# Optimization experiments

Hardware: AMD Instinct MI355X
Metric: run time of the kernel (lower is better)

Reference implementation:

```python
import jax, jax.numpy as jnp
import numpy as np

B, T, M, D, H, DK, DV = 2, 1024, 1024, 1024, 16, 64, 64
R = 2 * T + M  # number of relative positions required by rel_shift path


def setup_inputs() -> dict:
    key = jax.random.key(0)
    ks = jax.random.split(key, 11)
    s = 0.02
    return {
        "inputs": jax.random.normal(ks[0], (B, T, D), jnp.float32),
        "attention_mask": jnp.ones((B, T, M + T), jnp.float32),
        "positional_encodings": jax.random.normal(ks[1], (R, D), jnp.float32),
        "memory": jax.random.normal(ks[2], (B, M, D), jnp.float32),
        "Wq": jax.random.normal(ks[3], (D, H * DK), jnp.float32) * s,
        "Wk": jax.random.normal(ks[4], (D, H * DK), jnp.float32) * s,
        "Wv": jax.random.normal(ks[5], (D, H * DV), jnp.float32) * s,
        "Wr": jax.random.normal(ks[6], (D, H * DK), jnp.float32) * s,
        "r_w_bias": jax.random.normal(ks[7], (H, DK), jnp.float32) * s,
        "r_r_bias": jax.random.normal(ks[8], (H, DK), jnp.float32) * s,
        "W_out": jax.random.normal(ks[9], (H * DV, D), jnp.float32) * s,
    }


def _rel_shift(m, attention_length):
    # m: [T_q, T_q + L] -> [T_q, L], TXL relative shift via reshape/slice
    tq, total = m.shape
    x = m.reshape(total, tq)[1:].reshape(tq, total - 1)
    return x[:, :attention_length]


def reference(inputs, attention_mask, positional_encodings, memory,
              Wq, Wk, Wv, Wr, r_w_bias, r_r_bias, W_out):
    b, t, d = inputs.shape
    values = jnp.concatenate([memory, inputs], axis=1)  # [B, L, D]
    L = values.shape[1]
    q = (inputs @ Wq).reshape(b, t, H, DK)
    k = (values @ Wk).reshape(b, L, H, DK)
    v = (values @ Wv).reshape(b, L, H, DV)
    rk = (positional_encodings @ Wr).reshape(-1, H, DK)  # [R, H, DK]
    # content + relative logits (TXL)
    content = jnp.einsum('bthd,bThd->bhtT', q + r_w_bias, k)        # [B,H,T,L]
    rel = jnp.einsum('bthd,rhd->bhtr', q + r_r_bias, rk)            # [B,H,T,R]
    rel = jax.vmap(jax.vmap(lambda m: _rel_shift(m, L)))(rel)       # [B,H,T,L]
    logits = (content + rel) * (DK ** -0.5)
    masked = logits - (1.0 - attention_mask[:, None, :, :]) * 1e30
    w = jax.nn.softmax(masked, axis=-1)
    attn = jnp.einsum('bhtT,bThd->bthd', w, v)                      # [B,T,H,DV]
    return attn.reshape(b, t, H * DV) @ W_out
```

## Files before the change

### kernel.cpp

```cpp
#include <hip/hip_runtime.h>
#include <hip/hip_fp16.h>
#include <stdint.h>

#define Bz 2
#define Tq 1024
#define Mm 1024
#define Hh 16
#define Ll 2048
#define Rr 3072

typedef __attribute__((ext_vector_type(8))) short bf16x8;
typedef __attribute__((ext_vector_type(4))) float f32x4;

typedef __attribute__((address_space(3))) uint8_t lds_u8_t;
typedef __attribute__((address_space(1))) uint8_t glb_u8_t;

__device__ __forceinline__ void gl2lds16(const void* g, void* l) {
  __builtin_amdgcn_global_load_lds((const glb_u8_t*)g, (lds_u8_t*)l, 16, 0, 0);
}

__device__ __forceinline__ unsigned short f2bf(float f) {
  unsigned int u = __builtin_bit_cast(unsigned int, f);
  u = u + 0x7fffu + ((u >> 16) & 1u);
  return (unsigned short)(u >> 16);
}
__device__ __forceinline__ float b2f(unsigned short s) {
  unsigned int u = ((unsigned int)s) << 16;
  return __builtin_bit_cast(float, u);
}

__global__ __launch_bounds__(256) void k_prep2(
    const float* __restrict__ x, const float* __restrict__ mem,
    const float* __restrict__ pos, const float* __restrict__ mask,
    const float* __restrict__ w0, const float* __restrict__ w1,
    const float* __restrict__ w2, const float* __restrict__ w3,
    const float* __restrict__ w4,
    unsigned short* __restrict__ vin, unsigned short* __restrict__ pb,
    unsigned short* __restrict__ mb,
    unsigned short* __restrict__ t0, unsigned short* __restrict__ t1,
    unsigned short* __restrict__ t2, unsigned short* __restrict__ t3,
    unsigned short* __restrict__ t4) {
  __shared__ float tile[64][65];
  int bid = blockIdx.x;
  if (bid < 4096) {
    int idx = bid * 256 + threadIdx.x;
    int e = idx << 2;
    int row = e >> 10, col = e & 1023;
    int b = row >> 11, l = row & 2047;
    const float* s = (l < Mm) ? (mem + (((size_t)b * Mm + l) << 10) + col)
                              : (x + (((size_t)b * Tq + (l - Mm)) << 10) + col);
    float4 v = *(const float4*)s;
    ushort4 o;
    o.x = f2bf(v.x); o.y = f2bf(v.y); o.z = f2bf(v.z); o.w = f2bf(v.w);
    *(ushort4*)(vin + e) = o;
  } else if (bid < 7168) {
    int idx = (bid - 4096) * 256 + threadIdx.x;
    int e = idx << 2;
    float4 v = *(const float4*)(pos + e);
    ushort4 t;
    t.x = f2bf(v.x); t.y = f2bf(v.y); t.z = f2bf(v.z); t.w = f2bf(v.w);
    *(ushort4*)(pb + e) = t;
  } else if (bid < 11264) {
    int idx = (bid - 7168) * 256 + threadIdx.x;
    int e = idx << 2;
    const float BIGM = 1.442695e30f;
    float4 v = *(const float4*)(mask + e);
    ushort4 t;
    t.x = f2bf((1.0f - v.x) * BIGM); t.y = f2bf((1.0f - v.y) * BIGM);
    t.z = f2bf((1.0f - v.z) * BIGM); t.w = f2bf((1.0f - v.w) * BIGM);
    *(ushort4*)(mb + e) = t;
  } else {
    int r3 = bid - 11264;
    int mz = r3 >> 8, rem = r3 & 255;
    const float* W;
    unsigned short* WT;
    switch (mz) {
      case 0: W = w0; WT = t0; break;
      case 1: W = w1; WT = t1; break;
      case 2: W = w2; WT = t2; break;
      case 3: W = w3; WT = t3; break;
      default: W = w4; WT = t4; break;
    }
    int k0 = (rem >> 4) * 64, n0 = (rem & 15) * 64;
    int tid = threadIdx.x;
    int rr = tid >> 4, c4 = (tid & 15) * 4;
#pragma unroll
    for (int it = 0; it < 4; ++it) {
      int r = rr + it * 16;
      float4 v = *(const float4*)(W + (size_t)(k0 + r) * 1024 + n0 + c4);
      tile[r][c4] = v.x; tile[r][c4 + 1] = v.y;
      tile[r][c4 + 2] = v.z; tile[r][c4 + 3] = v.w;
    }
    __syncthreads();
#pragma unroll
    for (int it = 0; it < 4; ++it) {
      int n = rr + it * 16;
      ushort4 o;
      o.x = f2bf(tile[c4 + 0][n]); o.y = f2bf(tile[c4 + 1][n]);
      o.z = f2bf(tile[c4 + 2][n]); o.w = f2bf(tile[c4 + 3][n]);
      *(ushort4*)(WT + (size_t)(n0 + n) * 1024 + k0 + c4) = o;
    }
  }
}

template <int RMAP>
__device__ __forceinline__ void gemm_core(const unsigned short* __restrict__ A,
                                          const unsigned short* __restrict__ Bt,
                                          int m0, int n0, unsigned short* As,
                                          unsigned short* Bs, f32x4 acc[4][4]) {
  const int tid = threadIdx.x;
  const int w = tid >> 6, lane = tid & 63;
  const int quad = lane >> 4, li = lane & 15;
  const int wr = w >> 1, wc = w & 1;
  f32x4 z = {0.f, 0.f, 0.f, 0.f};
#pragma unroll
  for (int mi = 0; mi < 4; ++mi)
#pragma unroll
    for (int ni = 0; ni < 4; ++ni) acc[mi][ni] = z;

  const int rs = lane >> 2;
  const int cs = lane & 3;

  for (int k0 = 0; k0 < 1024; k0 += 32) {
    __syncthreads();
#pragma unroll
    for (int s = 0; s < 2; ++s) {
      int i = w * 2 + s;
      int r = i * 16 + rs;
      int c = cs ^ ((r >> 1) & 3);
      int ar = m0 + r;
      if (RMAP) ar = ar + 1024 + (ar & 1024);
      gl2lds16(A + (size_t)ar * 1024 + k0 + c * 8, (char*)As + i * 1024);
      int br = n0 + r;
      gl2lds16(Bt + (size_t)br * 1024 + k0 + c * 8, (char*)Bs + i * 1024);
    }
    __syncthreads();
    bf16x8 af[4], bfr[4];
#pragma unroll
    for (int mi = 0; mi < 4; ++mi) {
      int r = wr * 64 + mi * 16 + li;
      int ch = quad ^ ((r >> 1) & 3);
      af[mi] = *(const bf16x8*)((const char*)As + r * 64 + ch * 16);
    }
#pragma unroll
    for (int ni = 0; ni < 4; ++ni) {
      int r = wc * 64 + ni * 16 + li;
      int ch = quad ^ ((r >> 1) & 3);
      bfr[ni] = *(const bf16x8*)((const char*)Bs + r * 64 + ch * 16);
    }
#pragma unroll
    for (int mi = 0; mi < 4; ++mi)
#pragma unroll
      for (int ni = 0; ni < 4; ++ni)
        acc[mi][ni] = __builtin_amdgcn_mfma_f32_16x16x32_bf16(
            af[mi], bfr[ni], acc[mi][ni], 0, 0, 0);
  }
}

__global__ __launch_bounds__(256, 2) void k_proj(
    const unsigned short* __restrict__ Vin, const unsigned short* __restrict__ Pb,
    const unsigned short* __restrict__ WqT, const unsigned short* __restrict__ WkT,
    const unsigned short* __restrict__ WvT, const unsigned short* __restrict__ WrT,
    unsigned short* __restrict__ qb, unsigned short* __restrict__ kb,
    unsigned short* __restrict__ vtb, unsigned short* __restrict__ rkb) {
  __shared__ unsigned short As[128 * 32];
  __shared__ unsigned short Bs[128 * 32];
  __shared__ unsigned short Bs2[128 * 32];
  const int t = blockIdx.x;
  const int tid = threadIdx.x, w = tid >> 6, lane = tid & 63;
  const int quad = lane >> 4, li = lane & 15, wr = w >> 1, wc = w & 1;
  f32x4 z = {0.f, 0.f, 0.f, 0.f};

  if (t < 256) {
    int m0 = (t >> 3) * 128, n0 = (t & 7) * 128;
    f32x4 ak[4][4], av[4][4];
#pragma unroll
    for (int mi = 0; mi < 4; ++mi)
#pragma unroll
      for (int ni = 0; ni < 4; ++ni) { ak[mi][ni] = z; av[mi][ni] = z; }
    const int rs = lane >> 2, cs = lane & 3;
    for (int k0 = 0; k0 < 1024; k0 += 32) {
      __syncthreads();
#pragma unroll
      for (int s = 0; s < 2; ++s) {
        int i = w * 2 + s;
        int r = i * 16 + rs;
        int c = cs ^ ((r >> 1) & 3);
        gl2lds16(Vin + (size_t)(m0 + r) * 1024 + k0 + c * 8, (char*)As + i * 1024);
        gl2lds16(WkT + (size_t)(n0 + r) * 1024 + k0 + c * 8, (char*)Bs + i * 1024);
        gl2lds16(WvT + (size_t)(n0 + r) * 1024 + k0 + c * 8, (char*)Bs2 + i * 1024);
      }
      __syncthreads();
      bf16x8 af[4], bk[4], bv[4];
#pragma unroll
      for (int mi = 0; mi < 4; ++mi) {
        int r = wr * 64 + mi * 16 + li;
        int ch = quad ^ ((r >> 1) & 3);
        af[mi] = *(const bf16x8*)((const char*)As + r * 64 + ch * 16);
      }
#pragma unroll
      for (int ni = 0; ni < 4; ++ni) {
        int r = wc * 64 + ni * 16 + li;
        int ch = quad ^ ((r >> 1) & 3);
        bk[ni] = *(const bf16x8*)((const char*)Bs + r * 64 + ch * 16);
        bv[ni] = *(const bf16x8*)((const char*)Bs2 + r * 64 + ch * 16);
      }
#pragma unroll
      for (int mi = 0; mi < 4; ++mi)
#pragma unroll
        for (int ni = 0; ni < 4; ++ni) {
          ak[mi][ni] = __builtin_amdgcn_mfma_f32_16x16x32_bf16(
              af[mi], bk[ni], ak[mi][ni], 0, 0, 0);
          av[mi][ni] = __builtin_amdgcn_mfma_f32_16x16x32_bf16(
              af[mi], bv[ni], av[mi][ni], 0, 0, 0);
        }
    }
#pragma unroll
    for (int mi = 0; mi < 4; ++mi)
#pragma unroll
      for (int ni = 0; ni < 4; ++ni) {
        int cc = n0 + wc * 64 + ni * 16 + li;
#pragma unroll
        for (int reg = 0; reg < 4; ++reg) {
          int rrow = m0 + wr * 64 + mi * 16 + quad * 4 + reg;
          kb[(size_t)rrow * 1024 + cc] = f2bf(ak[mi][ni][reg]);
        }
        int r0 = m0 + wr * 64 + mi * 16 + quad * 4;
        int b = r0 >> 11, l0 = r0 & 2047;
        ushort4 o;
        o.x = f2bf(av[mi][ni][0]); o.y = f2bf(av[mi][ni][1]);
        o.z = f2bf(av[mi][ni][2]); o.w = f2bf(av[mi][ni][3]);
        *(ushort4*)(vtb + ((size_t)(b * 1024 + cc)) * Ll + l0) = o;
      }
  } else if (t < 384) {
    int tt = t - 256;
    int m0 = (tt >> 3) * 128, n0 = (tt & 7) * 128;
    f32x4 acc[4][4];
    gemm_core<1>(Vin, WqT, m0, n0, As, Bs, acc);
#pragma unroll
    for (int mi = 0; mi < 4; ++mi)
#pragma unroll
      for (int ni = 0; ni < 4; ++ni)
#pragma unroll
        for (int reg = 0; reg < 4; ++reg) {
          int rrow = m0 + wr * 64 + mi * 16 + quad * 4 + reg;
          int cc = n0 + wc * 64 + ni * 16 + li;
          qb[(size_t)rrow * 1024 + cc] = f2bf(acc[mi][ni][reg]);
        }
  } else {
    int tt = t - 384;
    int m0 = (tt >> 3) * 128, n0 = (tt & 7) * 128;
    f32x4 acc[4][4];
    gemm_core<0>(Pb, WrT, m0, n0, As, Bs, acc);
#pragma unroll
    for (int mi = 0; mi < 4; ++mi)
#pragma unroll
      for (int ni = 0; ni < 4; ++ni)
#pragma unroll
        for (int reg = 0; reg < 4; ++reg) {
          int rrow = m0 + wr * 64 + mi * 16 + quad * 4 + reg;
          int cc = n0 + wc * 64 + ni * 16 + li;
          rkb[(size_t)rrow * 1024 + cc] = f2bf(acc[mi][ni][reg]);
        }
  }
}

__global__ __launch_bounds__(256) void k_gemm_out64(
    const unsigned short* __restrict__ attnb, const unsigned short* __restrict__ WoT,
    float* __restrict__ out) {
  __shared__ unsigned short As[64 * 32];
  __shared__ unsigned short Bs[128 * 32];
  int m0 = blockIdx.x * 64, n0 = blockIdx.y * 128;
  const int tid = threadIdx.x, w = tid >> 6, lane = tid & 63;
  const int quad = lane >> 4, li = lane & 15, wr = w >> 1, wc = w & 1;
  f32x4 z = {0.f, 0.f, 0.f, 0.f};
  f32x4 acc[2][4];
#pragma unroll
  for (int mi = 0; mi < 2; ++mi)
#pragma unroll
    for (int ni = 0; ni < 4; ++ni) acc[mi][ni] = z;
  const int rs = lane >> 2, cs = lane & 3;
  for (int k0 = 0; k0 < 1024; k0 += 32) {
    __syncthreads();
    {
      int r = w * 16 + rs;
      int c = cs ^ ((r >> 1) & 3);
      gl2lds16(attnb + (size_t)(m0 + r) * 1024 + k0 + c * 8, (char*)As + w * 1024);
    }
#pragma unroll
    for (int s = 0; s < 2; ++s) {
      int i = w * 2 + s;
      int r = i * 16 + rs;
      int c = cs ^ ((r >> 1) & 3);
      gl2lds16(WoT + (size_t)(n0 + r) * 1024 + k0 + c * 8, (char*)Bs + i * 1024);
    }
    __syncthreads();
    bf16x8 af[2], bfr[4];
#pragma unroll
    for (int mi = 0; mi < 2; ++mi) {
      int r = wr * 32 + mi * 16 + li;
      int ch = quad ^ ((r >> 1) & 3);
      af[mi] = *(const bf16x8*)((const char*)As + r * 64 + ch * 16);
    }
#pragma unroll
    for (int ni = 0; ni < 4; ++ni) {
      int r = wc * 64 + ni * 16 + li;
      int ch = quad ^ ((r >> 1) & 3);
      bfr[ni] = *(const bf16x8*)((const char*)Bs + r * 64 + ch * 16);
    }
#pragma unroll
    for (int mi = 0; mi < 2; ++mi)
#pragma unroll
      for (int ni = 0; ni < 4; ++ni)
        acc[mi][ni] = __builtin_amdgcn_mfma_f32_16x16x32_bf16(
            af[mi], bfr[ni], acc[mi][ni], 0, 0, 0);
  }
#pragma unroll
  for (int mi = 0; mi < 2; ++mi)
#pragma unroll
    for (int ni = 0; ni < 4; ++ni)
#pragma unroll
      for (int reg = 0; reg < 4; ++reg) {
        int rrow = m0 + wr * 32 + mi * 16 + quad * 4 + reg;
        int cc = n0 + wc * 64 + ni * 16 + li;
        out[(size_t)rrow * 1024 + cc] = acc[mi][ni][reg];
      }
}

__global__ __launch_bounds__(256, 2) void k_attn(
    const unsigned short* __restrict__ qb, const float* __restrict__ rwb,
    const float* __restrict__ rrb,
    const unsigned short* __restrict__ kb, const unsigned short* __restrict__ vt,
    const unsigned short* __restrict__ rkb, const unsigned short* __restrict__ mb,
    unsigned short* __restrict__ attnb) {
  __shared__ unsigned short Ks[2][64 * 64];
  __shared__ unsigned short Vs[2][64 * 64];
  __shared__ unsigned short Rs[256 * 64];
  __shared__ unsigned short Sb[4][16 * 72];

  const int tid = threadIdx.x;
  const int w = tid >> 6, lane = tid & 63;
  const int quad = lane >> 4, li = lane & 15;
  const int qt = blockIdx.x, h = blockIdx.y, b = blockIdx.z;
  const int t0blk = qt * 64;
  const int t0w = t0blk + w * 16;
  const int rboff = 48 - 16 * w;
  const int rbase0 = Tq - t0blk - 63;

  bf16x8 aqw[2], aqr[2];
  {
    const unsigned short* p1 = qb + ((size_t)((b * Tq + t0w + li) * Hh + h)) * 64;
#pragma unroll
    for (int ks = 0; ks < 2; ++ks) {
      bf16x8 qf = *(const bf16x8*)(p1 + ks * 32 + quad * 8);
      const float* wp = rwb + h * 64 + ks * 32 + quad * 8;
      const float* rp = rrb + h * 64 + ks * 32 + quad * 8;
      float4 w0 = *(const float4*)wp, w1 = *(const float4*)(wp + 4);
      float4 r0 = *(const float4*)rp, r1 = *(const float4*)(rp + 4);
      float wv[8] = {w0.x, w0.y, w0.z, w0.w, w1.x, w1.y, w1.z, w1.w};
      float rv[8] = {r0.x, r0.y, r0.z, r0.w, r1.x, r1.y, r1.z, r1.w};
#pragma unroll
      for (int i2 = 0; i2 < 8; ++i2) {
        float qv = b2f((unsigned short)qf[i2]);
        aqw[ks][i2] = (short)f2bf(qv + wv[i2]);
        aqr[ks][i2] = (short)f2bf(qv + rv[i2]);
      }
    }
  }

  f32x4 z = {0.f, 0.f, 0.f, 0.f};
  f32x4 o[4];
  o[0] = z; o[1] = z; o[2] = z; o[3] = z;
  f32x4 ol = z;

  const int srow = lane >> 3;
  const int scs = lane & 7;
  const float SC = 0.125f * 1.4426950408889634f;
  const short oneb = 0x3F80;
  const bf16x8 onesf = {oneb, oneb, oneb, oneb, oneb, oneb, oneb, oneb};

  unsigned short* pw = &Sb[w][0];
  const unsigned short* mrowA = mb + ((size_t)(b * Tq + t0w + li)) * Ll;
  int srcl[4];
#pragma unroll
  for (int reg = 0; reg < 4; ++reg) {
    int row = quad * 4 + reg;
    srcl[reg] = (lane & 48) + ((li + row + 1) & 15);
  }

#pragma unroll
  for (int s = 0; s < 4; ++s) {
    int i = w * 4 + s;
    int r = i * 8 + srow;
    int gr = rbase0 + r;
    if (gr > Rr - 1) gr = Rr - 1;
    int c = scs ^ (r & 7);
    gl2lds16(rkb + ((size_t)gr * Hh + h) * 64 + c * 8, (char*)Rs + i * 1024);
  }
#pragma unroll
  for (int s = 0; s < 2; ++s) {
    int i = w * 2 + s;
    int r = i * 8 + srow;
    int c = scs ^ (r & 7);
    gl2lds16(kb + ((size_t)((b * Ll + r) * Hh + h)) * 64 + c * 8,
             (char*)Ks[0] + i * 1024);
    gl2lds16(vt + ((size_t)((b * Hh + h) * 64 + r)) * Ll + c * 8,
             (char*)Vs[0] + i * 1024);
  }

  for (int jt = 0; jt < 32; ++jt) {
    const int j0 = jt * 64;
    const int cur = jt & 1, nxt = cur ^ 1;
    __builtin_amdgcn_s_waitcnt(0x0F70);
    __syncthreads();
    bf16x8 mv0 = *(const bf16x8*)(mrowA + j0 + quad * 8);
    bf16x8 mv1 = *(const bf16x8*)(mrowA + j0 + 32 + quad * 8);
    asm volatile("" ::: "memory");
    if (jt < 31) {
      const int j0n = j0 + 64;
#pragma unroll
      for (int s = 0; s < 2; ++s) {
        int i = w * 2 + s;
        int r = i * 8 + srow;
        int c = scs ^ (r & 7);
        gl2lds16(kb + ((size_t)((b * Ll + j0n + r) * Hh + h)) * 64 + c * 8,
                 (char*)Ks[nxt] + i * 1024);
        gl2lds16(vt + ((size_t)((b * Hh + h) * 64 + r)) * Ll + j0n + c * 8,
                 (char*)Vs[nxt] + i * 1024);
      }
#pragma unroll
      for (int s = 0; s < 2; ++s) {
        int i2 = w * 2 + s;
        int rr = i2 * 8 + srow;
        int ofs = j0 + 128 + rr;
        int gr = rbase0 + ofs;
        if (gr > Rr - 1) gr = Rr - 1;
        int ring = ofs & 255;
        int c = scs ^ (rr & 7);
        gl2lds16(rkb + ((size_t)gr * Hh + h) * 64 + c * 8, (char*)Rs + ring * 128);
      }
    }
    const unsigned short* KsC = Ks[cur];
    const unsigned short* VsC = Vs[cur];
    f32x4 sc[4];
    sc[0] = z; sc[1] = z; sc[2] = z; sc[3] = z;
#pragma unroll
    for (int ks = 0; ks < 2; ++ks)
#pragma unroll
      for (int nt = 0; nt < 4; ++nt) {
        int j = nt * 16 + li;
        int ch = (ks * 4 + quad) ^ (j & 7);
        bf16x8 kf = *(const bf16x8*)((const char*)KsC + j * 128 + ch * 16);
        sc[nt] = __builtin_amdgcn_mfma_f32_16x16x32_bf16(aqw[ks], kf, sc[nt], 0, 0, 0);
      }
    f32x4 bd[5];
    bd[0] = z; bd[1] = z; bd[2] = z; bd[3] = z; bd[4] = z;
#pragma unroll
    for (int ks = 0; ks < 2; ++ks)
#pragma unroll
      for (int nt = 0; nt < 5; ++nt) {
        int pr = (rboff + nt * 16 + li + j0) & 255;
        int ch = (ks * 4 + quad) ^ (pr & 7);
        bf16x8 rf = *(const bf16x8*)((const char*)Rs + pr * 128 + ch * 16);
        bd[nt] = __builtin_amdgcn_mfma_f32_16x16x32_bf16(aqr[ks], rf, bd[nt], 0, 0, 0);
      }
    float rot[4][4];
#pragma unroll
    for (int nt = 0; nt < 4; ++nt)
#pragma unroll
      for (int reg = 0; reg < 4; ++reg)
        rot[nt][reg] = __shfl(sc[nt][reg], srcl[reg], 64);
#pragma unroll
    for (int nt = 0; nt < 5; ++nt)
#pragma unroll
      for (int reg = 0; reg < 4; ++reg) {
        int row = quad * 4 + reg;
        int jj = nt * 16 + li + row - 15;
        int ntlo = (nt == 0) ? 3 : (nt - 1);
        int nthi = (nt > 3) ? 0 : nt;
        float val = ((li + row) >= 15) ? rot[nthi][reg] : rot[ntlo][reg];
        float s = val + bd[nt][reg];
        if ((unsigned)jj < 64u)
          pw[row * 72 + jj] = __builtin_bit_cast(unsigned short, __float2half(s));
      }
    __builtin_amdgcn_s_waitcnt(0xc07f);
#pragma unroll
    for (int ks = 0; ks < 2; ++ks) {
      const int cofs = ks * 32 + quad * 8;
      ushort4 s0 = *(const ushort4*)(pw + li * 72 + cofs);
      ushort4 s1 = *(const ushort4*)(pw + li * 72 + cofs + 4);
      bf16x8 mv = ks ? mv1 : mv0;
      unsigned short su[8] = {s0.x, s0.y, s0.z, s0.w, s1.x, s1.y, s1.z, s1.w};
      bf16x8 ap;
#pragma unroll
      for (int i2 = 0; i2 < 8; ++i2) {
        float sf = __half2float(__builtin_bit_cast(__half, su[i2]));
        float mvf = b2f((unsigned short)mv[i2]);
        float p = exp2f(sf * SC - mvf);
        ap[i2] = (short)f2bf(p);
      }
      ol = __builtin_amdgcn_mfma_f32_16x16x32_bf16(ap, onesf, ol, 0, 0, 0);
#pragma unroll
      for (int nt = 0; nt < 4; ++nt) {
        int dv = nt * 16 + li;
        int ch = (ks * 4 + quad) ^ (dv & 7);
        bf16x8 vf = *(const bf16x8*)((const char*)VsC + dv * 128 + ch * 16);
        o[nt] = __builtin_amdgcn_mfma_f32_16x16x32_bf16(ap, vf, o[nt], 0, 0, 0);
      }
    }
  }
  float inv[4];
#pragma unroll
  for (int reg = 0; reg < 4; ++reg) inv[reg] = 1.0f / ol[reg];
#pragma unroll
  for (int nt = 0; nt < 4; ++nt)
#pragma unroll
    for (int reg = 0; reg < 4; ++reg) {
      int trow = t0w + quad * 4 + reg;
      attnb[((size_t)(b * Tq + trow)) * 1024 + h * 64 + nt * 16 + li] =
          f2bf(o[nt][reg] * inv[reg]);
    }
}

extern "C" void kernel_launch(void* const* d_in, const int* in_sizes, int n_in,
                              void* d_out, int out_size, void* d_ws, size_t ws_size,
                              hipStream_t stream) {
  const float* x = (const float*)d_in[0];
  const float* mask = (const float*)d_in[1];
  const float* pos = (const float*)d_in[2];
  const float* mem = (const float*)d_in[3];
  const float* Wq = (const float*)d_in[4];
  const float* Wk = (const float*)d_in[5];
  const float* Wv = (const float*)d_in[6];
  const float* Wr = (const float*)d_in[7];
  const float* rwb = (const float*)d_in[8];
  const float* rrb = (const float*)d_in[9];
  const float* Wo = (const float*)d_in[10];
  float* out = (float*)d_out;

  uint8_t* ws = (uint8_t*)d_ws;
  const size_t MB = 1024 * 1024;
  unsigned short* Vinb = (unsigned short*)(ws + 0);
  unsigned short* WqT = (unsigned short*)(ws + 8 * MB);
  unsigned short* WkT = (unsigned short*)(ws + 10 * MB);
  unsigned short* WvT = (unsigned short*)(ws + 12 * MB);
  unsigned short* WrT = (unsigned short*)(ws + 14 * MB);
  unsigned short* WoT = (unsigned short*)(ws + 16 * MB);
  unsigned short* Pb = (unsigned short*)(ws + 18 * MB);
  unsigned short* qb = (unsigned short*)(ws + 24 * MB);
  unsigned short* kb = (unsigned short*)(ws + 32 * MB);
  unsigned short* vtb = (unsigned short*)(ws + 40 * MB);
  unsigned short* rkb = (unsigned short*)(ws + 48 * MB);
  unsigned short* mbb = (unsigned short*)(ws + 54 * MB);
  unsigned short* attnb = (unsigned short*)(ws + 19 * MB);

  hipLaunchKernelGGL(k_prep2, dim3(12544), dim3(256), 0, stream,
                     x, mem, pos, mask, Wq, Wk, Wv, Wr, Wo,
                     Vinb, Pb, mbb, WqT, WkT, WvT, WrT, WoT);
  hipLaunchKernelGGL(k_proj, dim3(576), dim3(256), 0, stream,
                     Vinb, Pb, WqT, WkT, WvT, WrT, qb, kb, vtb, rkb);
  hipLaunchKernelGGL(k_attn, dim3(16, 16, 2), dim3(256), 0, stream,
                     qb, rwb, rrb, kb, vtb, rkb, mbb, attnb);
  hipLaunchKernelGGL(k_gemm_out64, dim3(32, 8), dim3(256), 0, stream,
                     attnb, WoT, out);
}
```

Measured before the change: 269.3 us.

## Double-buffer LDS tiles in projection and output GEMMs; split fused K/V blocks

The projection and output GEMMs now keep two LDS buffers. The next K-slice is prefetched with global_load_lds while MFMAs run on the current slice, so one barrier per step replaces the load/wait/compute sequence. The fused K+V projection blocks are split into separate K and V blocks with one accumulator set each, which raises the grid from 576 to 832 blocks. The minimum-occupancy hint is dropped. The aim is to hide global-load latency and add parallelism, at the cost of reading the shared A operand twice for K and V and using more LDS per block.

Result: faster. 262.1 us (-2.7%).

```diff
diff --git a/kernel.cpp b/kernel.cpp
--- a/kernel.cpp
+++ b/kernel.cpp
@@ -104,7 +104,7 @@
 }
 
 template <int RMAP>
-__device__ __forceinline__ void gemm_core(const unsigned short* __restrict__ A,
+__device__ __forceinline__ void gemm_pipe(const unsigned short* __restrict__ A,
                                           const unsigned short* __restrict__ Bt,
                                           int m0, int n0, unsigned short* As,
                                           unsigned short* Bs, f32x4 acc[4][4]) {
@@ -121,32 +121,48 @@
   const int rs = lane >> 2;
   const int cs = lane & 3;
 
+#pragma unroll
+  for (int s = 0; s < 2; ++s) {
+    int i = w * 2 + s;
+    int r = i * 16 + rs;
+    int c = cs ^ ((r >> 1) & 3);
+    int ar = m0 + r;
+    if (RMAP) ar = ar + 1024 + (ar & 1024);
+    gl2lds16(A + (size_t)ar * 1024 + c * 8, (char*)As + i * 1024);
+    gl2lds16(Bt + (size_t)(n0 + r) * 1024 + c * 8, (char*)Bs + i * 1024);
+  }
+
   for (int k0 = 0; k0 < 1024; k0 += 32) {
+    const int bo = ((k0 >> 5) & 1) * 8192;
+    const int no = bo ^ 8192;
+    __builtin_amdgcn_s_waitcnt(0x0F70);
     __syncthreads();
-#pragma unroll
-    for (int s = 0; s < 2; ++s) {
-      int i = w * 2 + s;
-      int r = i * 16 + rs;
-      int c = cs ^ ((r >> 1) & 3);
-      int ar = m0 + r;
-      if (RMAP) ar = ar + 1024 + (ar & 1024);
-      gl2lds16(A + (size_t)ar * 1024 + k0 + c * 8, (char*)As + i * 1024);
-      int br = n0 + r;
-      gl2lds16(Bt + (size_t)br * 1024 + k0 + c * 8, (char*)Bs + i * 1024);
-    }
-    __syncthreads();
+    if (k0 + 32 < 1024) {
+#pragma unroll
+      for (int s = 0; s < 2; ++s) {
+        int i = w * 2 + s;
+        int r = i * 16 + rs;
+        int c = cs ^ ((r >> 1) & 3);
+        int ar = m0 + r;
+        if (RMAP) ar = ar + 1024 + (ar & 1024);
+        gl2lds16(A + (size_t)ar * 1024 + k0 + 32 + c * 8,
+                 (char*)As + no + i * 1024);
+        gl2lds16(Bt + (size_t)(n0 + r) * 1024 + k0 + 32 + c * 8,
+                 (char*)Bs + no + i * 1024);
+      }
+    }
     bf16x8 af[4], bfr[4];
 #pragma unroll
     for (int mi = 0; mi < 4; ++mi) {
       int r = wr * 64 + mi * 16 + li;
       int ch = quad ^ ((r >> 1) & 3);
-      af[mi] = *(const bf16x8*)((const char*)As + r * 64 + ch * 16);
+      af[mi] = *(const bf16x8*)((const char*)As + bo + r * 64 + ch * 16);
     }
 #pragma unroll
     for (int ni = 0; ni < 4; ++ni) {
       int r = wc * 64 + ni * 16 + li;
       int ch = quad ^ ((r >> 1) & 3);
-      bfr[ni] = *(const bf16x8*)((const char*)Bs + r * 64 + ch * 16);
+      bfr[ni] = *(const bf16x8*)((const char*)Bs + bo + r * 64 + ch * 16);
     }
 #pragma unroll
     for (int mi = 0; mi < 4; ++mi)
@@ -157,86 +173,52 @@
   }
 }
 
-__global__ __launch_bounds__(256, 2) void k_proj(
+__global__ __launch_bounds__(256) void k_proj(
     const unsigned short* __restrict__ Vin, const unsigned short* __restrict__ Pb,
     const unsigned short* __restrict__ WqT, const unsigned short* __restrict__ WkT,
     const unsigned short* __restrict__ WvT, const unsigned short* __restrict__ WrT,
     unsigned short* __restrict__ qb, unsigned short* __restrict__ kb,
     unsigned short* __restrict__ vtb, unsigned short* __restrict__ rkb) {
-  __shared__ unsigned short As[128 * 32];
-  __shared__ unsigned short Bs[128 * 32];
-  __shared__ unsigned short Bs2[128 * 32];
+  __shared__ unsigned short As[2 * 128 * 32];
+  __shared__ unsigned short Bs[2 * 128 * 32];
   const int t = blockIdx.x;
   const int tid = threadIdx.x, w = tid >> 6, lane = tid & 63;
   const int quad = lane >> 4, li = lane & 15, wr = w >> 1, wc = w & 1;
-  f32x4 z = {0.f, 0.f, 0.f, 0.f};
+  f32x4 acc[4][4];
 
   if (t < 256) {
     int m0 = (t >> 3) * 128, n0 = (t & 7) * 128;
-    f32x4 ak[4][4], av[4][4];
+    gemm_pipe<0>(Vin, WkT, m0, n0, As, Bs, acc);
 #pragma unroll
     for (int mi = 0; mi < 4; ++mi)
 #pragma unroll
-      for (int ni = 0; ni < 4; ++ni) { ak[mi][ni] = z; av[mi][ni] = z; }
-    const int rs = lane >> 2, cs = lane & 3;
-    for (int k0 = 0; k0 < 1024; k0 += 32) {
-      __syncthreads();
-#pragma unroll
-      for (int s = 0; s < 2; ++s) {
-        int i = w * 2 + s;
-        int r = i * 16 + rs;
-        int c = cs ^ ((r >> 1) & 3);
-        gl2lds16(Vin + (size_t)(m0 + r) * 1024 + k0 + c * 8, (char*)As + i * 1024);
-        gl2lds16(WkT + (size_t)(n0 + r) * 1024 + k0 + c * 8, (char*)Bs + i * 1024);
-        gl2lds16(WvT + (size_t)(n0 + r) * 1024 + k0 + c * 8, (char*)Bs2 + i * 1024);
-      }
-      __syncthreads();
-      bf16x8 af[4], bk[4], bv[4];
-#pragma unroll
-      for (int mi = 0; mi < 4; ++mi) {
-        int r = wr * 64 + mi * 16 + li;
-        int ch = quad ^ ((r >> 1) & 3);
-        af[mi] = *(const bf16x8*)((const char*)As + r * 64 + ch * 16);
-      }
-#pragma unroll
-      for (int ni = 0; ni < 4; ++ni) {
-        int r = wc * 64 + ni * 16 + li;
-        int ch = quad ^ ((r >> 1) & 3);
-        bk[ni] = *(const bf16x8*)((const char*)Bs + r * 64 + ch * 16);
-        bv[ni] = *(const bf16x8*)((const char*)Bs2 + r * 64 + ch * 16);
-      }
-#pragma unroll
-      for (int mi = 0; mi < 4; ++mi)
-#pragma unroll
-        for (int ni = 0; ni < 4; ++ni) {
-          ak[mi][ni] = __builtin_amdgcn_mfma_f32_16x16x32_bf16(
-              af[mi], bk[ni], ak[mi][ni], 0, 0, 0);
-          av[mi][ni] = __builtin_amdgcn_mfma_f32_16x16x32_bf16(
-              af[mi], bv[ni], av[mi][ni], 0, 0, 0);
-        }
-    }
-#pragma unroll
-    for (int mi = 0; mi < 4; ++mi)
-#pragma unroll
-      for (int ni = 0; ni < 4; ++ni) {
-        int cc = n0 + wc * 64 + ni * 16 + li;
+      for (int ni = 0; ni < 4; ++ni)
 #pragma unroll
         for (int reg = 0; reg < 4; ++reg) {
           int rrow = m0 + wr * 64 + mi * 16 + quad * 4 + reg;
-          kb[(size_t)rrow * 1024 + cc] = f2bf(ak[mi][ni][reg]);
+          int cc = n0 + wc * 64 + ni * 16 + li;
+          kb[(size_t)rrow * 1024 + cc] = f2bf(acc[mi][ni][reg]);
         }
+  } else if (t < 512) {
+    int tt = t - 256;
+    int m0 = (tt >> 3) * 128, n0 = (tt & 7) * 128;
+    gemm_pipe<0>(Vin, WvT, m0, n0, As, Bs, acc);
+#pragma unroll
+    for (int mi = 0; mi < 4; ++mi)
+#pragma unroll
+      for (int ni = 0; ni < 4; ++ni) {
         int r0 = m0 + wr * 64 + mi * 16 + quad * 4;
         int b = r0 >> 11, l0 = r0 & 2047;
+        int cc = n0 + wc * 64 + ni * 16 + li;
         ushort4 o;
-        o.x = f2bf(av[mi][ni][0]); o.y = f2bf(av[mi][ni][1]);
-        o.z = f2bf(av[mi][ni][2]); o.w = f2bf(av[mi][ni][3]);
+        o.x = f2bf(acc[mi][ni][0]); o.y = f2bf(acc[mi][ni][1]);
+        o.z = f2bf(acc[mi][ni][2]); o.w = f2bf(acc[mi][ni][3]);
         *(ushort4*)(vtb + ((size_t)(b * 1024 + cc)) * Ll + l0) = o;
       }
-  } else if (t < 384) {
-    int tt = t - 256;
+  } else if (t < 640) {
+    int tt = t - 512;
     int m0 = (tt >> 3) * 128, n0 = (tt & 7) * 128;
-    f32x4 acc[4][4];
-    gemm_core<1>(Vin, WqT, m0, n0, As, Bs, acc);
+    gemm_pipe<1>(Vin, WqT, m0, n0, As, Bs, acc);
 #pragma unroll
     for (int mi = 0; mi < 4; ++mi)
 #pragma unroll
@@ -248,10 +230,9 @@
           qb[(size_t)rrow * 1024 + cc] = f2bf(acc[mi][ni][reg]);
         }
   } else {
-    int tt = t - 384;
+    int tt = t - 640;
     int m0 = (tt >> 3) * 128, n0 = (tt & 7) * 128;
-    f32x4 acc[4][4];
-    gemm_core<0>(Pb, WrT, m0, n0, As, Bs, acc);
+    gemm_pipe<0>(Pb, WrT, m0, n0, As, Bs, acc);
 #pragma unroll
     for (int mi = 0; mi < 4; ++mi)
 #pragma unroll
@@ -268,8 +249,8 @@
 __global__ __launch_bounds__(256) void k_gemm_out64(
     const unsigned short* __restrict__ attnb, const unsigned short* __restrict__ WoT,
     float* __restrict__ out) {
-  __shared__ unsigned short As[64 * 32];
-  __shared__ unsigned short Bs[128 * 32];
+  __shared__ unsigned short As[2 * 64 * 32];
+  __shared__ unsigned short Bs[2 * 128 * 32];
   int m0 = blockIdx.x * 64, n0 = blockIdx.y * 128;
   const int tid = threadIdx.x, w = tid >> 6, lane = tid & 63;
   const int quad = lane >> 4, li = lane & 15, wr = w >> 1, wc = w & 1;
@@ -280,33 +261,53 @@
 #pragma unroll
     for (int ni = 0; ni < 4; ++ni) acc[mi][ni] = z;
   const int rs = lane >> 2, cs = lane & 3;
+
+  {
+    int r = w * 16 + rs;
+    int c = cs ^ ((r >> 1) & 3);
+    gl2lds16(attnb + (size_t)(m0 + r) * 1024 + c * 8, (char*)As + w * 1024);
+  }
+#pragma unroll
+  for (int s = 0; s < 2; ++s) {
+    int i = w * 2 + s;
+    int r = i * 16 + rs;
+    int c = cs ^ ((r >> 1) & 3);
+    gl2lds16(WoT + (size_t)(n0 + r) * 1024 + c * 8, (char*)Bs + i * 1024);
+  }
+
   for (int k0 = 0; k0 < 1024; k0 += 32) {
+    const int boa = ((k0 >> 5) & 1) * 4096;
+    const int bob = ((k0 >> 5) & 1) * 8192;
+    __builtin_amdgcn_s_waitcnt(0x0F70);
     __syncthreads();
-    {
-      int r = w * 16 + rs;
-      int c = cs ^ ((r >> 1) & 3);
-      gl2lds16(attnb + (size_t)(m0 + r) * 1024 + k0 + c * 8, (char*)As + w * 1024);
-    }
-#pragma unroll
-    for (int s = 0; s < 2; ++s) {
-      int i = w * 2 + s;
-      int r = i * 16 + rs;
-      int c = cs ^ ((r >> 1) & 3);
-      gl2lds16(WoT + (size_t)(n0 + r) * 1024 + k0 + c * 8, (char*)Bs + i * 1024);
-    }
-    __syncthreads();
+    if (k0 + 32 < 1024) {
+      {
+        int r = w * 16 + rs;
+        int c = cs ^ ((r >> 1) & 3);
+        gl2lds16(attnb + (size_t)(m0 + r) * 1024 + k0 + 32 + c * 8,
+                 (char*)As + (boa ^ 4096) + w * 1024);
+      }
+#pragma unroll
+      for (int s = 0; s < 2; ++s) {
+        int i = w * 2 + s;
+        int r = i * 16 + rs;
+        int c = cs ^ ((r >> 1) & 3);
+        gl2lds16(WoT + (size_t)(n0 + r) * 1024 + k0 + 32 + c * 8,
+                 (char*)Bs + (bob ^ 8192) + i * 1024);
+      }
+    }
     bf16x8 af[2], bfr[4];
 #pragma unroll
     for (int mi = 0; mi < 2; ++mi) {
       int r = wr * 32 + mi * 16 + li;
       int ch = quad ^ ((r >> 1) & 3);
-      af[mi] = *(const bf16x8*)((const char*)As + r * 64 + ch * 16);
+      af[mi] = *(const bf16x8*)((const char*)As + boa + r * 64 + ch * 16);
     }
 #pragma unroll
     for (int ni = 0; ni < 4; ++ni) {
       int r = wc * 64 + ni * 16 + li;
       int ch = quad ^ ((r >> 1) & 3);
-      bfr[ni] = *(const bf16x8*)((const char*)Bs + r * 64 + ch * 16);
+      bfr[ni] = *(const bf16x8*)((const char*)Bs + bob + r * 64 + ch * 16);
     }
 #pragma unroll
     for (int mi = 0; mi < 2; ++mi)
@@ -557,7 +558,7 @@
   hipLaunchKernelGGL(k_prep2, dim3(12544), dim3(256), 0, stream,
                      x, mem, pos, mask, Wq, Wk, Wv, Wr, Wo,
                      Vinb, Pb, mbb, WqT, WkT, WvT, WrT, WoT);
-  hipLaunchKernelGGL(k_proj, dim3(576), dim3(256), 0, stream,
+  hipLaunchKernelGGL(k_proj, dim3(832), dim3(256), 0, stream,
                      Vinb, Pb, WqT, WkT, WvT, WrT, qb, kb, vtb, rkb);
   hipLaunchKernelGGL(k_attn, dim3(16, 16, 2), dim3(256), 0, stream,
                      qb, rwb, rrb, kb, vtb, rkb, mbb, attnb);
```
